# Kernel tuning notes

Measured on AMD Instinct MI355X. Metric: run time of the kernel, lower is better.

Reference implementation:

```python
import jax, jax.numpy as jnp
import numpy as np

N = 50000      # nodes
E = 1600000    # edges
IN = 128       # in_features
OUT = 64       # out_features
H = 2          # heads
ALPHA = 0.2    # LeakyReLU negative slope


def setup_inputs() -> dict:
    key = jax.random.key(0)
    k1, k2, k3, k4 = jax.random.split(key, 4)
    x = jax.random.normal(k1, (N, IN), dtype=jnp.float32)
    edge_index = jax.random.randint(k2, (2, E), 0, N, dtype=jnp.int32)
    # xavier-uniform-ish scaled params
    W = jax.random.normal(k3, (H, IN, OUT), dtype=jnp.float32) / np.float32(np.sqrt(IN))
    a = jax.random.normal(k4, (H, 2 * OUT, 1), dtype=jnp.float32) * np.float32(0.1)
    return {"x": x, "W": W, "a": a, "edge_index": edge_index}


def reference(x, W, a, edge_index):
    src = edge_index[0]
    dst = edge_index[1]
    # per-head linear transform: [N, H, O]
    Wh = jnp.einsum('ni,hio->nho', x, W)
    # split attention vector: a @ [Wh_i || Wh_j] == Wh_i@a_i + Wh_j@a_j
    a_i = a[:, :OUT, 0]   # [H, O]
    a_j = a[:, OUT:, 0]   # [H, O]
    s_i = jnp.einsum('nho,ho->nh', Wh, a_i)   # [N, H]
    s_j = jnp.einsum('nho,ho->nh', Wh, a_j)   # [N, H]
    # per-edge attention logits, LeakyReLU
    e = jax.nn.leaky_relu(s_i[src] + s_j[dst], negative_slope=ALPHA)  # [E, H]
    # faithful to source: GLOBAL softmax over all edges (dim=0) per head
    attn = jax.nn.softmax(e, axis=0)  # [E, H]
    # dropout with rate 0.0 -> identity (eval mode)
    msg = attn[:, :, None] * Wh[dst]  # [E, H, O]
    h = jax.ops.segment_sum(msg, dst, num_segments=N)  # [N, H, O]
    # concat heads along feature dim
    return h.reshape(N, H * OUT)
```

## Files before the change

### kernel.cpp

```cpp
#include <hip/hip_runtime.h>

#define NN 50000
#define EE 1600000
#define INF 128
#define OUTF 64
#define NH 2
#define ALPHA 0.2f

#define NSPREP 391
#define NWPREP 64
#define NBNODE 391

#define HCH 32
#define RNG 8
#define NPR (NN / RNG)
#define EPC (EE / HCH)
#define NI4 (EPC / 4)
#define HWAVES 16
#define WITER ((NI4 + 1023) / 1024)
#define QW 512

typedef __attribute__((ext_vector_type(8))) short s16x8;
typedef __attribute__((ext_vector_type(4))) float f32x4;

__device__ __forceinline__ unsigned short bf16_rne(float f) {
    union { float f; unsigned u; } v; v.f = f;
    unsigned r = v.u + 0x7FFFu + ((v.u >> 16) & 1u);
    return (unsigned short)(r >> 16);
}
__device__ __forceinline__ float bf16_val(unsigned short h) {
    union { unsigned u; float f; } v; v.u = ((unsigned)h) << 16;
    return v.f;
}
__device__ __forceinline__ void split8(const float4 a, const float4 b,
                                       s16x8& hi, s16x8& lo) {
    const float p[8] = {a.x, a.y, a.z, a.w, b.x, b.y, b.z, b.w};
    #pragma unroll
    for (int j = 0; j < 8; ++j) {
        const unsigned short h = bf16_rne(p[j]);
        hi[j] = (short)h;
        lo[j] = (short)bf16_rne(p[j] - bf16_val(h));
    }
}


__global__ __launch_bounds__(256)
void gat_prep(const float* __restrict__ x, const float* __restrict__ Wg,
              const float* __restrict__ av,
              float* __restrict__ si, float* __restrict__ sj,
              unsigned short* __restrict__ Wf, float* __restrict__ Z)
{
    __shared__ float4 u4[128];
    const int tid = threadIdx.x;

    if (blockIdx.x >= NSPREP) {
        const int idx = (blockIdx.x - NSPREP) * 256 + tid;
        if (idx < 2) Z[idx] = 0.0f;
        const int h = idx >> 13;
        const int k = (idx >> 6) & 127;
        const int o = idx & 63;
        const float w = Wg[idx];
        const unsigned short hi = bf16_rne(w);
        const unsigned short lo = bf16_rne(w - bf16_val(hi));
        const int n  = h * 64 + o;
        const int nt = n >> 4;
        const int ks = k >> 5;
        const int kk = k & 31;
        const int ln = (kk >> 3) * 16 + (n & 15);
        const int pos = ((nt * 4 + ks) * 64 + ln) * 8 + (kk & 7);
        Wf[pos] = hi;
        Wf[16384 + pos] = lo;
        return;
    }

    if (tid < 128) {
        const int k = tid;
        float u0 = 0.f, u1 = 0.f, u2 = 0.f, u3 = 0.f;
        #pragma unroll 4
        for (int o = 0; o < 64; o += 4) {
            const float4 w0 = *(const float4*)&Wg[k * 64 + o];
            const float4 w1 = *(const float4*)&Wg[8192 + k * 64 + o];
            const float4 ai0 = *(const float4*)&av[o];
            const float4 aj0 = *(const float4*)&av[64 + o];
            const float4 ai1 = *(const float4*)&av[128 + o];
            const float4 aj1 = *(const float4*)&av[192 + o];
            u0 += w0.x*ai0.x + w0.y*ai0.y + w0.z*ai0.z + w0.w*ai0.w;
            u1 += w0.x*aj0.x + w0.y*aj0.y + w0.z*aj0.z + w0.w*aj0.w;
            u2 += w1.x*ai1.x + w1.y*ai1.y + w1.z*ai1.z + w1.w*ai1.w;
            u3 += w1.x*aj1.x + w1.y*aj1.y + w1.z*aj1.z + w1.w*aj1.w;
        }
        u4[k] = make_float4(u0, u1, u2, u3);
    }
    __syncthreads();

    const int lane = tid & 63;
    const int wv = tid >> 6;
    const int lm = lane & 15;
    const int rsub = lane >> 4;

    #pragma unroll
    for (int p = 0; p < 8; ++p) {
        const int row = blockIdx.x * 128 + p * 16 + wv * 4 + rsub;
        const int rc = row < NN ? row : NN - 1;
        const float4 xa = *(const float4*)(x + (size_t)rc * INF + lm * 8);
        const float4 xb = *(const float4*)(x + (size_t)rc * INF + lm * 8 + 4);
        float s0 = 0.f, s1 = 0.f, s2 = 0.f, s3 = 0.f;
        const float xv[8] = {xa.x, xa.y, xa.z, xa.w, xb.x, xb.y, xb.z, xb.w};
        #pragma unroll
        for (int j = 0; j < 8; ++j) {
            const float4 u = u4[lm * 8 + j];
            s0 = fmaf(xv[j], u.x, s0);
            s1 = fmaf(xv[j], u.y, s1);
            s2 = fmaf(xv[j], u.z, s2);
            s3 = fmaf(xv[j], u.w, s3);
        }
        #pragma unroll
        for (int m = 1; m < 16; m <<= 1) {
            s0 += __shfl_xor(s0, m, 64);
            s1 += __shfl_xor(s1, m, 64);
            s2 += __shfl_xor(s2, m, 64);
            s3 += __shfl_xor(s3, m, 64);
        }
        if (lm == 0 && row < NN) {
            *(float2*)&si[2 * row] = make_float2(s0, s2);
            *(float2*)&sj[2 * row] = make_float2(s1, s3);
        }
    }
}

__global__ __launch_bounds__(1024)
void gat_hist(const int* __restrict__ ei,
              const float* __restrict__ si, const float* __restrict__ sj,
              float* __restrict__ partial, float* __restrict__ Z)
{
    __shared__ float bins[NPR * 2];
    __shared__ unsigned q[HWAVES * QW];
    __shared__ float zr0[HWAVES], zr1[HWAVES];
    const int c = blockIdx.x;
    const int r = blockIdx.y;
    const int nlo = r * NPR;
    const int tid = threadIdx.x;
    const int lane = tid & 63;
    const int wv = tid >> 6;
    const int qbase = wv * QW;

    for (int i = tid; i < NPR; i += 1024)
        ((float2*)bins)[i] = make_float2(0.f, 0.f);
    __syncthreads();

    const int4* src4 = (const int4*)(ei + (size_t)c * EPC);
    const int4* dst4 = (const int4*)(ei + EE + (size_t)c * EPC);

    float z0 = 0.f, z1 = 0.f;
    int qn = 0;

    for (int j = 0; j < WITER; ++j) {
        const int i = j * 1024 + tid;
        int4 d4 = make_int4(-1, -1, -1, -1);
        int4 s4 = make_int4(0, 0, 0, 0);
        if (i < NI4) { d4 = dst4[i]; s4 = src4[i]; }
        const unsigned dd[4] = {(unsigned)d4.x, (unsigned)d4.y,
                                (unsigned)d4.z, (unsigned)d4.w};
        const unsigned ss[4] = {(unsigned)s4.x, (unsigned)s4.y,
                                (unsigned)s4.z, (unsigned)s4.w};

        unsigned rel[4]; bool pass[4];
        #pragma unroll
        for (int k = 0; k < 4; ++k) {
            const unsigned rr = dd[k] / (unsigned)NPR;
            pass[k] = (rr == (unsigned)r);
            rel[k] = dd[k] - rr * (unsigned)NPR;
        }
        unsigned long long m[4];
        #pragma unroll
        for (int k = 0; k < 4; ++k) m[k] = __ballot(pass[k]);

        int cbase = qn;
        #pragma unroll
        for (int k = 0; k < 4; ++k) {
            const unsigned pre = __builtin_amdgcn_mbcnt_hi(
                (unsigned)(m[k] >> 32),
                __builtin_amdgcn_mbcnt_lo((unsigned)(m[k] & 0xffffffffu), 0u));
            if (pass[k])
                q[qbase + cbase + (int)pre] = ss[k] | (rel[k] << 16);
            cbase += __popcll(m[k]);
        }
        qn = cbase;

        if (qn > QW - 256 || j == WITER - 1) {
            for (int t = lane; t < qn; t += 64) {
                const unsigned pk = q[qbase + t];
                const int s = (int)(pk & 0xFFFFu);
                const int rl = (int)(pk >> 16);
                const float2 vi = *(const float2*)&si[2 * s];
                const float2 vj = *(const float2*)&sj[2 * (nlo + rl)];
                float a0 = vi.x + vj.x; a0 = a0 > 0.f ? a0 : ALPHA * a0;
                float a1 = vi.y + vj.y; a1 = a1 > 0.f ? a1 : ALPHA * a1;
                const float w0 = expf(a0);
                const float w1 = expf(a1);
                atomicAdd(&bins[2 * rl], w0);
                atomicAdd(&bins[2 * rl + 1], w1);
                z0 += w0; z1 += w1;
            }
            qn = 0;
        }
    }

    #pragma unroll
    for (int m = 1; m < 64; m <<= 1) {
        z0 += __shfl_xor(z0, m, 64);
        z1 += __shfl_xor(z1, m, 64);
    }
    if (lane == 0) { zr0[wv] = z0; zr1[wv] = z1; }
    __syncthreads();
    if (tid == 0) {
        float t0 = 0.f, t1 = 0.f;
        #pragma unroll
        for (int i = 0; i < HWAVES; ++i) { t0 += zr0[i]; t1 += zr1[i]; }
        atomicAdd(&Z[0], t0);
        atomicAdd(&Z[1], t1);
    }

    float2* P = (float2*)(partial + (size_t)c * 100000 + 2 * nlo);
    for (int i = tid; i < NPR; i += 1024)
        P[i] = ((const float2*)bins)[i];
}

__global__ __launch_bounds__(256)
void gat_node(const float* __restrict__ x, const unsigned short* __restrict__ Wf,
              const float* __restrict__ partial, const float* __restrict__ Z,
              float* __restrict__ out)
{
    __shared__ unsigned short WsL[32768];
    __shared__ float asum[256];
    const int tid = threadIdx.x;
    const int lane = tid & 63;
    const int wv = tid >> 6;
    const int lm = lane & 15;
    const int quad = lane >> 4;

    {
        const float4* gsrc = (const float4*)Wf;
        float4* ldst = (float4*)WsL;
        #pragma unroll
        for (int i = 0; i < 16; ++i)
            ldst[i * 256 + tid] = gsrc[i * 256 + tid];
    }

    {
        const int vbase = blockIdx.x * 256;
        float s = 0.f;
        if (vbase + tid < 2 * NN) {
            #pragma unroll
            for (int cc = 0; cc < HCH; ++cc)
                s += partial[(size_t)cc * 100000 + vbase + tid];
        }
        asum[tid] = s;
    }

    const float rz0 = 1.0f / Z[0];
    const float rz1 = 1.0f / Z[1];

    const int rowA0 = blockIdx.x * 128 + wv * 32 + lm;
    const int rowA1 = rowA0 + 16;
    const int rc0 = rowA0 < NN ? rowA0 : NN - 1;
    const int rc1 = rowA1 < NN ? rowA1 : NN - 1;
    const float* xp0 = x + (size_t)rc0 * INF + quad * 8;
    const float* xp1 = x + (size_t)rc1 * INF + quad * 8;

    f32x4 acc[2][8];
    #pragma unroll
    for (int mi = 0; mi < 2; ++mi)
        #pragma unroll
        for (int nt = 0; nt < 8; ++nt) acc[mi][nt] = (f32x4)0.0f;

    __syncthreads();

    #pragma unroll
    for (int ks = 0; ks < 4; ++ks) {
        s16x8 ah0, al0, ah1, al1;
        {
            const float4 u0 = *(const float4*)(xp0 + ks * 32);
            const float4 v0 = *(const float4*)(xp0 + ks * 32 + 4);
            split8(u0, v0, ah0, al0);
            const float4 u1 = *(const float4*)(xp1 + ks * 32);
            const float4 v1 = *(const float4*)(xp1 + ks * 32 + 4);
            split8(u1, v1, ah1, al1);
        }
        #pragma unroll
        for (int nt = 0; nt < 8; ++nt) {
            const s16x8 bh = *(const s16x8*)&WsL[((nt * 4 + ks) * 64 + lane) * 8];
            const s16x8 bl = *(const s16x8*)&WsL[16384 + ((nt * 4 + ks) * 64 + lane) * 8];
            acc[0][nt] = __builtin_amdgcn_mfma_f32_16x16x32_bf16(ah0, bh, acc[0][nt], 0, 0, 0);
            acc[0][nt] = __builtin_amdgcn_mfma_f32_16x16x32_bf16(ah0, bl, acc[0][nt], 0, 0, 0);
            acc[0][nt] = __builtin_amdgcn_mfma_f32_16x16x32_bf16(al0, bh, acc[0][nt], 0, 0, 0);
            acc[1][nt] = __builtin_amdgcn_mfma_f32_16x16x32_bf16(ah1, bh, acc[1][nt], 0, 0, 0);
            acc[1][nt] = __builtin_amdgcn_mfma_f32_16x16x32_bf16(ah1, bl, acc[1][nt], 0, 0, 0);
            acc[1][nt] = __builtin_amdgcn_mfma_f32_16x16x32_bf16(al1, bh, acc[1][nt], 0, 0, 0);
        }
    }

    #pragma unroll
    for (int mi = 0; mi < 2; ++mi) {
        const int rowoffb = wv * 32 + mi * 16 + quad * 4;
        const int rowb = blockIdx.x * 128 + rowoffb;
        #pragma unroll
        for (int r = 0; r < 4; ++r) {
            const int rr = rowb + r;
            if (rr < NN) {
                const float sc0 = asum[2 * (rowoffb + r)] * rz0;
                const float sc1 = asum[2 * (rowoffb + r) + 1] * rz1;
                float* orow = out + (size_t)rr * (NH * OUTF) + lm;
                #pragma unroll
                for (int nt = 0; nt < 8; ++nt)
                    orow[nt * 16] = acc[mi][nt][r] * (nt < 4 ? sc0 : sc1);
            }
        }
    }
}

extern "C" void kernel_launch(void* const* d_in, const int* in_sizes, int n_in,
                              void* d_out, int out_size, void* d_ws, size_t ws_size,
                              hipStream_t stream)
{
    const float* x = (const float*)d_in[0];
    const float* W = (const float*)d_in[1];
    const float* a = (const float*)d_in[2];
    const int* ei = (const int*)d_in[3];
    float* out = (float*)d_out;
    float* ws = (float*)d_ws;

    float* si = ws;
    float* sj = ws + 100000;
    float* Z = ws + 200000;
    unsigned short* Wf = (unsigned short*)(ws + 200064);
    float* partial = ws + 216448;

    gat_prep<<<dim3(NSPREP + NWPREP), dim3(256), 0, stream>>>(
        x, W, a, si, sj, Wf, Z);

    gat_hist<<<dim3(HCH, RNG), dim3(1024), 0, stream>>>(ei, si, sj, partial, Z);

    gat_node<<<dim3(NBNODE), dim3(256), 0, stream>>>(x, Wf, partial, Z, out);
}
```

Before: 140.9 us.

## Fuse prep, histogram and node kernels into one cooperative kernel with grid syncs

Replaces three separate kernel launches with a single cooperative kernel of 256 blocks of 1024 threads, using grid.sync between the score/weight prep, edge histogram and node GEMM phases. Shared memory is reused across phases through one buffer. This removes the launch gaps and per-kernel ramp-up and tail between stages. In exchange, the prep and node phases now run on only 256 large blocks, which may lower occupancy, and grid-wide barriers add their own cost.

Result: slower. 207.9 us (+47.5%).

```diff
diff --git a/kernel.cpp b/kernel.cpp
--- a/kernel.cpp
+++ b/kernel.cpp
@@ -1,4 +1,5 @@
 #include <hip/hip_runtime.h>
+#include <hip/hip_cooperative_groups.h>
 
 #define NN 50000
 #define EE 1600000
@@ -7,17 +8,16 @@
 #define NH 2
 #define ALPHA 0.2f
 
-#define NSPREP 391
-#define NWPREP 64
-#define NBNODE 391
+#define NBLK 256
+#define NTHR 1024
+#define NWAVE 16
 
 #define HCH 32
 #define RNG 8
 #define NPR (NN / RNG)
 #define EPC (EE / HCH)
 #define NI4 (EPC / 4)
-#define HWAVES 16
-#define WITER ((NI4 + 1023) / 1024)
+#define WITER ((NI4 + NTHR - 1) / NTHR)
 #define QW 512
 
 typedef __attribute__((ext_vector_type(8))) short s16x8;
@@ -44,276 +44,256 @@
 }
 
 
-__global__ __launch_bounds__(256)
-void gat_prep(const float* __restrict__ x, const float* __restrict__ Wg,
-              const float* __restrict__ av,
-              float* __restrict__ si, float* __restrict__ sj,
-              unsigned short* __restrict__ Wf, float* __restrict__ Z)
+__global__ __launch_bounds__(NTHR)
+void gat_fused(const float* __restrict__ x, const float* __restrict__ Wg,
+               const float* __restrict__ av, const int* __restrict__ ei,
+               float* __restrict__ si, float* __restrict__ sj,
+               unsigned short* __restrict__ Wf, float* __restrict__ partial,
+               float* __restrict__ Z, float* __restrict__ out)
 {
-    __shared__ float4 u4[128];
-    const int tid = threadIdx.x;
-
-    if (blockIdx.x >= NSPREP) {
-        const int idx = (blockIdx.x - NSPREP) * 256 + tid;
-        if (idx < 2) Z[idx] = 0.0f;
-        const int h = idx >> 13;
-        const int k = (idx >> 6) & 127;
-        const int o = idx & 63;
-        const float w = Wg[idx];
-        const unsigned short hi = bf16_rne(w);
-        const unsigned short lo = bf16_rne(w - bf16_val(hi));
-        const int n  = h * 64 + o;
-        const int nt = n >> 4;
-        const int ks = k >> 5;
-        const int kk = k & 31;
-        const int ln = (kk >> 3) * 16 + (n & 15);
-        const int pos = ((nt * 4 + ks) * 64 + ln) * 8 + (kk & 7);
-        Wf[pos] = hi;
-        Wf[16384 + pos] = lo;
-        return;
-    }
-
-    if (tid < 128) {
-        const int k = tid;
-        float u0 = 0.f, u1 = 0.f, u2 = 0.f, u3 = 0.f;
-        #pragma unroll 4
-        for (int o = 0; o < 64; o += 4) {
-            const float4 w0 = *(const float4*)&Wg[k * 64 + o];
-            const float4 w1 = *(const float4*)&Wg[8192 + k * 64 + o];
-            const float4 ai0 = *(const float4*)&av[o];
-            const float4 aj0 = *(const float4*)&av[64 + o];
-            const float4 ai1 = *(const float4*)&av[128 + o];
-            const float4 aj1 = *(const float4*)&av[192 + o];
-            u0 += w0.x*ai0.x + w0.y*ai0.y + w0.z*ai0.z + w0.w*ai0.w;
-            u1 += w0.x*aj0.x + w0.y*aj0.y + w0.z*aj0.z + w0.w*aj0.w;
-            u2 += w1.x*ai1.x + w1.y*ai1.y + w1.z*ai1.z + w1.w*ai1.w;
-            u3 += w1.x*aj1.x + w1.y*aj1.y + w1.z*aj1.z + w1.w*aj1.w;
-        }
-        u4[k] = make_float4(u0, u1, u2, u3);
-    }
-    __syncthreads();
-
-    const int lane = tid & 63;
-    const int wv = tid >> 6;
-    const int lm = lane & 15;
-    const int rsub = lane >> 4;
-
-    #pragma unroll
-    for (int p = 0; p < 8; ++p) {
-        const int row = blockIdx.x * 128 + p * 16 + wv * 4 + rsub;
-        const int rc = row < NN ? row : NN - 1;
-        const float4 xa = *(const float4*)(x + (size_t)rc * INF + lm * 8);
-        const float4 xb = *(const float4*)(x + (size_t)rc * INF + lm * 8 + 4);
-        float s0 = 0.f, s1 = 0.f, s2 = 0.f, s3 = 0.f;
-        const float xv[8] = {xa.x, xa.y, xa.z, xa.w, xb.x, xb.y, xb.z, xb.w};
-        #pragma unroll
-        for (int j = 0; j < 8; ++j) {
-            const float4 u = u4[lm * 8 + j];
-            s0 = fmaf(xv[j], u.x, s0);
-            s1 = fmaf(xv[j], u.y, s1);
-            s2 = fmaf(xv[j], u.z, s2);
-            s3 = fmaf(xv[j], u.w, s3);
-        }
-        #pragma unroll
-        for (int m = 1; m < 16; m <<= 1) {
-            s0 += __shfl_xor(s0, m, 64);
-            s1 += __shfl_xor(s1, m, 64);
-            s2 += __shfl_xor(s2, m, 64);
-            s3 += __shfl_xor(s3, m, 64);
-        }
-        if (lm == 0 && row < NN) {
-            *(float2*)&si[2 * row] = make_float2(s0, s2);
-            *(float2*)&sj[2 * row] = make_float2(s1, s3);
-        }
-    }
-}
-
-__global__ __launch_bounds__(1024)
-void gat_hist(const int* __restrict__ ei,
-              const float* __restrict__ si, const float* __restrict__ sj,
-              float* __restrict__ partial, float* __restrict__ Z)
-{
-    __shared__ float bins[NPR * 2];
-    __shared__ unsigned q[HWAVES * QW];
-    __shared__ float zr0[HWAVES], zr1[HWAVES];
-    const int c = blockIdx.x;
-    const int r = blockIdx.y;
-    const int nlo = r * NPR;
+    namespace cg = cooperative_groups;
+    cg::grid_group grid = cg::this_grid();
+
+    __shared__ __align__(16) char smem[83968];
+    __shared__ float zr0[NWAVE], zr1[NWAVE];
+
+    const int bid = blockIdx.x;
     const int tid = threadIdx.x;
     const int lane = tid & 63;
     const int wv = tid >> 6;
-    const int qbase = wv * QW;
-
-    for (int i = tid; i < NPR; i += 1024)
-        ((float2*)bins)[i] = make_float2(0.f, 0.f);
-    __syncthreads();
-
-    const int4* src4 = (const int4*)(ei + (size_t)c * EPC);
-    const int4* dst4 = (const int4*)(ei + EE + (size_t)c * EPC);
-
-    float z0 = 0.f, z1 = 0.f;
-    int qn = 0;
-
-    for (int j = 0; j < WITER; ++j) {
-        const int i = j * 1024 + tid;
-        int4 d4 = make_int4(-1, -1, -1, -1);
-        int4 s4 = make_int4(0, 0, 0, 0);
-        if (i < NI4) { d4 = dst4[i]; s4 = src4[i]; }
-        const unsigned dd[4] = {(unsigned)d4.x, (unsigned)d4.y,
-                                (unsigned)d4.z, (unsigned)d4.w};
-        const unsigned ss[4] = {(unsigned)s4.x, (unsigned)s4.y,
-                                (unsigned)s4.z, (unsigned)s4.w};
-
-        unsigned rel[4]; bool pass[4];
+
+    {
+        float4* u4 = (float4*)smem;
+        if (tid < 128) {
+            const int k = tid;
+            float u0 = 0.f, u1 = 0.f, u2 = 0.f, u3 = 0.f;
+            #pragma unroll 4
+            for (int o = 0; o < 64; o += 4) {
+                const float4 w0 = *(const float4*)&Wg[k * 64 + o];
+                const float4 w1 = *(const float4*)&Wg[8192 + k * 64 + o];
+                const float4 ai0 = *(const float4*)&av[o];
+                const float4 aj0 = *(const float4*)&av[64 + o];
+                const float4 ai1 = *(const float4*)&av[128 + o];
+                const float4 aj1 = *(const float4*)&av[192 + o];
+                u0 += w0.x*ai0.x + w0.y*ai0.y + w0.z*ai0.z + w0.w*ai0.w;
+                u1 += w0.x*aj0.x + w0.y*aj0.y + w0.z*aj0.z + w0.w*aj0.w;
+                u2 += w1.x*ai1.x + w1.y*ai1.y + w1.z*ai1.z + w1.w*ai1.w;
+                u3 += w1.x*aj1.x + w1.y*aj1.y + w1.z*aj1.z + w1.w*aj1.w;
+            }
+            u4[k] = make_float4(u0, u1, u2, u3);
+        }
+        __syncthreads();
+
+        if (bid * 256 < NN) {
+            const int lm = lane & 15;
+            const int rsub = lane >> 4;
+            #pragma unroll
+            for (int p = 0; p < 4; ++p) {
+                const int row = bid * 256 + wv * 16 + p * 4 + rsub;
+                const int rc = row < NN ? row : NN - 1;
+                const float4 xa = *(const float4*)(x + (size_t)rc * INF + lm * 8);
+                const float4 xb = *(const float4*)(x + (size_t)rc * INF + lm * 8 + 4);
+                float s0 = 0.f, s1 = 0.f, s2 = 0.f, s3 = 0.f;
+                const float xv[8] = {xa.x, xa.y, xa.z, xa.w, xb.x, xb.y, xb.z, xb.w};
+                #pragma unroll
+                for (int j = 0; j < 8; ++j) {
+                    const float4 u = u4[lm * 8 + j];
+                    s0 = fmaf(xv[j], u.x, s0);
+                    s1 = fmaf(xv[j], u.y, s1);
+                    s2 = fmaf(xv[j], u.z, s2);
+                    s3 = fmaf(xv[j], u.w, s3);
+                }
+                #pragma unroll
+                for (int m = 1; m < 16; m <<= 1) {
+                    s0 += __shfl_xor(s0, m, 64);
+                    s1 += __shfl_xor(s1, m, 64);
+                    s2 += __shfl_xor(s2, m, 64);
+                    s3 += __shfl_xor(s3, m, 64);
+                }
+                if (lm == 0 && row < NN) {
+                    *(float2*)&si[2 * row] = make_float2(s0, s2);
+                    *(float2*)&sj[2 * row] = make_float2(s1, s3);
+                }
+            }
+        }
+
+        if (bid < 16) {
+            const int idx = bid * 1024 + tid;
+            const int h = idx >> 13;
+            const int k = (idx >> 6) & 127;
+            const int o = idx & 63;
+            const float w = Wg[idx];
+            const unsigned short hi = bf16_rne(w);
+            const unsigned short lo = bf16_rne(w - bf16_val(hi));
+            const int n  = h * 64 + o;
+            const int nt = n >> 4;
+            const int ks = k >> 5;
+            const int kk = k & 31;
+            const int ln = (kk >> 3) * 16 + (n & 15);
+            const int pos = ((nt * 4 + ks) * 64 + ln) * 8 + (kk & 7);
+            Wf[pos] = hi;
+            Wf[16384 + pos] = lo;
+        }
+        if (bid == 0 && tid < 2) Z[tid] = 0.0f;
+    }
+
+    grid.sync();
+
+    {
+        float* bins = (float*)smem;
+        unsigned* q = (unsigned*)(smem + 50000);
+        const int c = bid & 31;
+        const int r = bid >> 5;
+        const int nlo = r * NPR;
+        const int qbase = wv * QW;
+
+        for (int i = tid; i < NPR; i += NTHR)
+            ((float2*)bins)[i] = make_float2(0.f, 0.f);
+        __syncthreads();
+
+        const int4* src4 = (const int4*)(ei + (size_t)c * EPC);
+        const int4* dst4 = (const int4*)(ei + EE + (size_t)c * EPC);
+
+        float z0 = 0.f, z1 = 0.f;
+        int qn = 0;
+
+        for (int j = 0; j < WITER; ++j) {
+            const int i = j * NTHR + tid;
+            int4 d4 = make_int4(-1, -1, -1, -1);
+            int4 s4 = make_int4(0, 0, 0, 0);
+            if (i < NI4) { d4 = dst4[i]; s4 = src4[i]; }
+            const unsigned dd[4] = {(unsigned)d4.x, (unsigned)d4.y,
+                                    (unsigned)d4.z, (unsigned)d4.w};
+            const unsigned ss[4] = {(unsigned)s4.x, (unsigned)s4.y,
+                                    (unsigned)s4.z, (unsigned)s4.w};
+
+            unsigned rel[4]; bool pass[4];
+            #pragma unroll
+            for (int k = 0; k < 4; ++k) {
+                const unsigned rr = dd[k] / (unsigned)NPR;
+                pass[k] = (rr == (unsigned)r);
+                rel[k] = dd[k] - rr * (unsigned)NPR;
+            }
+            unsigned long long m[4];
+            #pragma unroll
+            for (int k = 0; k < 4; ++k) m[k] = __ballot(pass[k]);
+
+            int cbase = qn;
+            #pragma unroll
+            for (int k = 0; k < 4; ++k) {
+                const unsigned pre = __builtin_amdgcn_mbcnt_hi(
+                    (unsigned)(m[k] >> 32),
+                    __builtin_amdgcn_mbcnt_lo((unsigned)(m[k] & 0xffffffffu), 0u));
+                if (pass[k])
+                    q[qbase + cbase + (int)pre] = ss[k] | (rel[k] << 16);
+                cbase += __popcll(m[k]);
+            }
+            qn = cbase;
+
+            if (qn > QW - 256 || j == WITER - 1) {
+                for (int t = lane; t < qn; t += 64) {
+                    const unsigned pk = q[qbase + t];
+                    const int s = (int)(pk & 0xFFFFu);
+                    const int rl = (int)(pk >> 16);
+                    const float2 vi = *(const float2*)&si[2 * s];
+                    const float2 vj = *(const float2*)&sj[2 * (nlo + rl)];
+                    float a0 = vi.x + vj.x; a0 = a0 > 0.f ? a0 : ALPHA * a0;
+                    float a1 = vi.y + vj.y; a1 = a1 > 0.f ? a1 : ALPHA * a1;
+                    const float w0 = expf(a0);
+                    const float w1 = expf(a1);
+                    atomicAdd(&bins[2 * rl], w0);
+                    atomicAdd(&bins[2 * rl + 1], w1);
+                    z0 += w0; z1 += w1;
+                }
+                qn = 0;
+            }
+        }
+
         #pragma unroll
-        for (int k = 0; k < 4; ++k) {
-            const unsigned rr = dd[k] / (unsigned)NPR;
-            pass[k] = (rr == (unsigned)r);
-            rel[k] = dd[k] - rr * (unsigned)NPR;
-        }
-        unsigned long long m[4];
-        #pragma unroll
-        for (int k = 0; k < 4; ++k) m[k] = __ballot(pass[k]);
-
-        int cbase = qn;
-        #pragma unroll
-        for (int k = 0; k < 4; ++k) {
-            const unsigned pre = __builtin_amdgcn_mbcnt_hi(
-                (unsigned)(m[k] >> 32),
-                __builtin_amdgcn_mbcnt_lo((unsigned)(m[k] & 0xffffffffu), 0u));
-            if (pass[k])
-                q[qbase + cbase + (int)pre] = ss[k] | (rel[k] << 16);
-            cbase += __popcll(m[k]);
-        }
-        qn = cbase;
-
-        if (qn > QW - 256 || j == WITER - 1) {
-            for (int t = lane; t < qn; t += 64) {
-                const unsigned pk = q[qbase + t];
-                const int s = (int)(pk & 0xFFFFu);
-                const int rl = (int)(pk >> 16);
-                const float2 vi = *(const float2*)&si[2 * s];
-                const float2 vj = *(const float2*)&sj[2 * (nlo + rl)];
-                float a0 = vi.x + vj.x; a0 = a0 > 0.f ? a0 : ALPHA * a0;
-                float a1 = vi.y + vj.y; a1 = a1 > 0.f ? a1 : ALPHA * a1;
-                const float w0 = expf(a0);
-                const float w1 = expf(a1);
-                atomicAdd(&bins[2 * rl], w0);
-                atomicAdd(&bins[2 * rl + 1], w1);
-                z0 += w0; z1 += w1;
-            }
-            qn = 0;
-        }
+        for (int m = 1; m < 64; m <<= 1) {
+            z0 += __shfl_xor(z0, m, 64);
+            z1 += __shfl_xor(z1, m, 64);
+        }
+        if (lane == 0) { zr0[wv] = z0; zr1[wv] = z1; }
+        __syncthreads();
+        if (tid == 0) {
+            float t0 = 0.f, t1 = 0.f;
+            #pragma unroll
+            for (int i = 0; i < NWAVE; ++i) { t0 += zr0[i]; t1 += zr1[i]; }
+            atomicAdd(&Z[0], t0);
+            atomicAdd(&Z[1], t1);
+        }
+
+        float2* P = (float2*)(partial + (size_t)c * 100000 + 2 * nlo);
+        for (int i = tid; i < NPR; i += NTHR)
+            P[i] = ((const float2*)bins)[i];
     }
 
-    #pragma unroll
-    for (int m = 1; m < 64; m <<= 1) {
-        z0 += __shfl_xor(z0, m, 64);
-        z1 += __shfl_xor(z1, m, 64);
-    }
-    if (lane == 0) { zr0[wv] = z0; zr1[wv] = z1; }
-    __syncthreads();
-    if (tid == 0) {
-        float t0 = 0.f, t1 = 0.f;
-        #pragma unroll
-        for (int i = 0; i < HWAVES; ++i) { t0 += zr0[i]; t1 += zr1[i]; }
-        atomicAdd(&Z[0], t0);
-        atomicAdd(&Z[1], t1);
-    }
-
-    float2* P = (float2*)(partial + (size_t)c * 100000 + 2 * nlo);
-    for (int i = tid; i < NPR; i += 1024)
-        P[i] = ((const float2*)bins)[i];
-}
-
-__global__ __launch_bounds__(256)
-void gat_node(const float* __restrict__ x, const unsigned short* __restrict__ Wf,
-              const float* __restrict__ partial, const float* __restrict__ Z,
-              float* __restrict__ out)
-{
-    __shared__ unsigned short WsL[32768];
-    __shared__ float asum[256];
-    const int tid = threadIdx.x;
-    const int lane = tid & 63;
-    const int wv = tid >> 6;
-    const int lm = lane & 15;
-    const int quad = lane >> 4;
+    grid.sync();
 
     {
-        const float4* gsrc = (const float4*)Wf;
-        float4* ldst = (float4*)WsL;
-        #pragma unroll
-        for (int i = 0; i < 16; ++i)
-            ldst[i * 256 + tid] = gsrc[i * 256 + tid];
-    }
-
-    {
-        const int vbase = blockIdx.x * 256;
-        float s = 0.f;
-        if (vbase + tid < 2 * NN) {
-            #pragma unroll
-            for (int cc = 0; cc < HCH; ++cc)
-                s += partial[(size_t)cc * 100000 + vbase + tid];
-        }
-        asum[tid] = s;
-    }
-
-    const float rz0 = 1.0f / Z[0];
-    const float rz1 = 1.0f / Z[1];
-
-    const int rowA0 = blockIdx.x * 128 + wv * 32 + lm;
-    const int rowA1 = rowA0 + 16;
-    const int rc0 = rowA0 < NN ? rowA0 : NN - 1;
-    const int rc1 = rowA1 < NN ? rowA1 : NN - 1;
-    const float* xp0 = x + (size_t)rc0 * INF + quad * 8;
-    const float* xp1 = x + (size_t)rc1 * INF + quad * 8;
-
-    f32x4 acc[2][8];
-    #pragma unroll
-    for (int mi = 0; mi < 2; ++mi)
-        #pragma unroll
-        for (int nt = 0; nt < 8; ++nt) acc[mi][nt] = (f32x4)0.0f;
-
-    __syncthreads();
-
-    #pragma unroll
-    for (int ks = 0; ks < 4; ++ks) {
-        s16x8 ah0, al0, ah1, al1;
+        unsigned short* Ws = (unsigned short*)smem;
+        float* asum = (float*)(smem + 65536);
+
         {
-            const float4 u0 = *(const float4*)(xp0 + ks * 32);
-            const float4 v0 = *(const float4*)(xp0 + ks * 32 + 4);
-            split8(u0, v0, ah0, al0);
-            const float4 u1 = *(const float4*)(xp1 + ks * 32);
-            const float4 v1 = *(const float4*)(xp1 + ks * 32 + 4);
-            split8(u1, v1, ah1, al1);
-        }
-        #pragma unroll
-        for (int nt = 0; nt < 8; ++nt) {
-            const s16x8 bh = *(const s16x8*)&WsL[((nt * 4 + ks) * 64 + lane) * 8];
-            const s16x8 bl = *(const s16x8*)&WsL[16384 + ((nt * 4 + ks) * 64 + lane) * 8];
-            acc[0][nt] = __builtin_amdgcn_mfma_f32_16x16x32_bf16(ah0, bh, acc[0][nt], 0, 0, 0);
-            acc[0][nt] = __builtin_amdgcn_mfma_f32_16x16x32_bf16(ah0, bl, acc[0][nt], 0, 0, 0);
-            acc[0][nt] = __builtin_amdgcn_mfma_f32_16x16x32_bf16(al0, bh, acc[0][nt], 0, 0, 0);
-            acc[1][nt] = __builtin_amdgcn_mfma_f32_16x16x32_bf16(ah1, bh, acc[1][nt], 0, 0, 0);
-            acc[1][nt] = __builtin_amdgcn_mfma_f32_16x16x32_bf16(ah1, bl, acc[1][nt], 0, 0, 0);
-            acc[1][nt] = __builtin_amdgcn_mfma_f32_16x16x32_bf16(al1, bh, acc[1][nt], 0, 0, 0);
-        }
-    }
-
-    #pragma unroll
-    for (int mi = 0; mi < 2; ++mi) {
-        const int rowoffb = wv * 32 + mi * 16 + quad * 4;
-        const int rowb = blockIdx.x * 128 + rowoffb;
-        #pragma unroll
-        for (int r = 0; r < 4; ++r) {
-            const int rr = rowb + r;
-            if (rr < NN) {
-                const float sc0 = asum[2 * (rowoffb + r)] * rz0;
-                const float sc1 = asum[2 * (rowoffb + r) + 1] * rz1;
+            const float4* gsrc = (const float4*)Wf;
+            float4* ldst = (float4*)Ws;
+            #pragma unroll
+            for (int i = 0; i < 4; ++i)
+                ldst[i * 1024 + tid] = gsrc[i * 1024 + tid];
+        }
+
+        if (tid < 512) {
+            const int vb = bid * 512 + tid;
+            float s = 0.f;
+            if (vb < 2 * NN) {
+                #pragma unroll
+                for (int cc = 0; cc < HCH; ++cc)
+                    s += partial[(size_t)cc * 100000 + vb];
+            }
+            asum[tid] = s;
+        }
+        __syncthreads();
+
+        const float rz0 = 1.0f / Z[0];
+        const float rz1 = 1.0f / Z[1];
+
+        const int w0 = bid * 256 + wv * 16;
+        if (w0 < NN) {
+            const int lm = lane & 15;
+            const int quad = lane >> 4;
+            const float* xp = x + (size_t)(w0 + lm) * INF + quad * 8;
+
+            f32x4 acc[8];
+            #pragma unroll
+            for (int nt = 0; nt < 8; ++nt) acc[nt] = (f32x4)0.0f;
+
+            #pragma unroll
+            for (int ks = 0; ks < 4; ++ks) {
+                s16x8 ah, al;
+                const float4 u = *(const float4*)(xp + ks * 32);
+                const float4 v = *(const float4*)(xp + ks * 32 + 4);
+                split8(u, v, ah, al);
+                #pragma unroll
+                for (int nt = 0; nt < 8; ++nt) {
+                    const s16x8 bh = *(const s16x8*)&Ws[((nt * 4 + ks) * 64 + lane) * 8];
+                    const s16x8 bl = *(const s16x8*)&Ws[16384 + ((nt * 4 + ks) * 64 + lane) * 8];
+                    acc[nt] = __builtin_amdgcn_mfma_f32_16x16x32_bf16(ah, bh, acc[nt], 0, 0, 0);
+                    acc[nt] = __builtin_amdgcn_mfma_f32_16x16x32_bf16(ah, bl, acc[nt], 0, 0, 0);
+                    acc[nt] = __builtin_amdgcn_mfma_f32_16x16x32_bf16(al, bh, acc[nt], 0, 0, 0);
+                }
+            }
+
+            const int lrow0 = wv * 16 + quad * 4;
+            #pragma unroll
+            for (int r = 0; r < 4; ++r) {
+                const int rr = bid * 256 + lrow0 + r;
+                const float sc0 = asum[2 * (lrow0 + r)] * rz0;
+                const float sc1 = asum[2 * (lrow0 + r) + 1] * rz1;
                 float* orow = out + (size_t)rr * (NH * OUTF) + lm;
                 #pragma unroll
                 for (int nt = 0; nt < 8; ++nt)
-                    orow[nt * 16] = acc[mi][nt][r] * (nt < 4 ? sc0 : sc1);
+                    orow[nt * 16] = acc[nt][r] * (nt < 4 ? sc0 : sc1);
             }
         }
     }
@@ -336,10 +316,9 @@
     unsigned short* Wf = (unsigned short*)(ws + 200064);
     float* partial = ws + 216448;
 
-    gat_prep<<<dim3(NSPREP + NWPREP), dim3(256), 0, stream>>>(
-        x, W, a, si, sj, Wf, Z);
-
-    gat_hist<<<dim3(HCH, RNG), dim3(1024), 0, stream>>>(ei, si, sj, partial, Z);
-
-    gat_node<<<dim3(NBNODE), dim3(256), 0, stream>>>(x, Wf, partial, Z, out);
-}
+    void* args[] = { (void*)&x, (void*)&W, (void*)&a, (void*)&ei,
+                     (void*)&si, (void*)&sj, (void*)&Wf, (void*)&partial,
+                     (void*)&Z, (void*)&out };
+    hipLaunchCooperativeKernel((const void*)gat_fused, dim3(NBLK), dim3(NTHR),
+                               args, 0, stream);
+}
```

## Prefetch next edge indices, replace division with range check, double hist chunks

Applied to the files above, without the earlier changes.

The histogram kernel now issues the global loads for the next iteration's edge indices before processing the current batch. This hides load latency behind the ballot, compaction and drain work. The per-edge integer division that found the destination range is replaced by a single unsigned subtract-and-compare against this block's node range. The edge dimension is split into twice as many chunks, each handled by 512-thread blocks, to give more blocks and better latency tolerance. In exchange, the partial-sum buffer doubles, so the node kernel reads and reduces twice as many partials per node.

After: 147.1 us. +4.4%, slower.

```diff
diff --git a/kernel.cpp b/kernel.cpp
--- a/kernel.cpp
+++ b/kernel.cpp
@@ -11,13 +11,13 @@
 #define NWPREP 64
 #define NBNODE 391
 
-#define HCH 32
+#define HCH 64
 #define RNG 8
 #define NPR (NN / RNG)
 #define EPC (EE / HCH)
 #define NI4 (EPC / 4)
-#define HWAVES 16
-#define WITER ((NI4 + 1023) / 1024)
+#define HWAVES 8
+#define WITER ((NI4 + 511) / 512)
 #define QW 512
 
 typedef __attribute__((ext_vector_type(8))) short s16x8;
@@ -128,7 +128,23 @@
     }
 }
 
-__global__ __launch_bounds__(1024)
+#define DRAIN_Q                                                         \
+    for (int t = lane; t < qn; t += 64) {                               \
+        const unsigned pk = q[qbase + t];                               \
+        const int s = (int)(pk & 0xFFFFu);                              \
+        const int rl = (int)(pk >> 16);                                 \
+        const float2 vi = *(const float2*)&si[2 * s];                   \
+        const float2 vj = *(const float2*)&sj[2 * (nlo + rl)];          \
+        float a0 = vi.x + vj.x; a0 = a0 > 0.f ? a0 : ALPHA * a0;        \
+        float a1 = vi.y + vj.y; a1 = a1 > 0.f ? a1 : ALPHA * a1;        \
+        const float w0 = expf(a0);                                      \
+        const float w1 = expf(a1);                                      \
+        atomicAdd(&bins[2 * rl], w0);                                   \
+        atomicAdd(&bins[2 * rl + 1], w1);                               \
+        z0 += w0; z1 += w1;                                             \
+    }
+
+__global__ __launch_bounds__(512)
 void gat_hist(const int* __restrict__ ei,
               const float* __restrict__ si, const float* __restrict__ sj,
               float* __restrict__ partial, float* __restrict__ Z)
@@ -139,12 +155,13 @@
     const int c = blockIdx.x;
     const int r = blockIdx.y;
     const int nlo = r * NPR;
+    const unsigned nlo_u = (unsigned)nlo;
     const int tid = threadIdx.x;
     const int lane = tid & 63;
     const int wv = tid >> 6;
     const int qbase = wv * QW;
 
-    for (int i = tid; i < NPR; i += 1024)
+    for (int i = tid; i < NPR; i += 512)
         ((float2*)bins)[i] = make_float2(0.f, 0.f);
     __syncthreads();
 
@@ -154,57 +171,45 @@
     float z0 = 0.f, z1 = 0.f;
     int qn = 0;
 
+    int4 d4 = make_int4(-1, -1, -1, -1);
+    int4 s4 = make_int4(0, 0, 0, 0);
+    if (tid < NI4) { d4 = dst4[tid]; s4 = src4[tid]; }
+
     for (int j = 0; j < WITER; ++j) {
-        const int i = j * 1024 + tid;
-        int4 d4 = make_int4(-1, -1, -1, -1);
-        int4 s4 = make_int4(0, 0, 0, 0);
-        if (i < NI4) { d4 = dst4[i]; s4 = src4[i]; }
+        int4 d4n = make_int4(-1, -1, -1, -1);
+        int4 s4n = make_int4(0, 0, 0, 0);
+        const int inx = (j + 1) * 512 + tid;
+        if (j + 1 < WITER && inx < NI4) { d4n = dst4[inx]; s4n = src4[inx]; }
+
+        if (qn >= QW - 256) {
+            DRAIN_Q;
+            qn = 0;
+        }
+
         const unsigned dd[4] = {(unsigned)d4.x, (unsigned)d4.y,
                                 (unsigned)d4.z, (unsigned)d4.w};
         const unsigned ss[4] = {(unsigned)s4.x, (unsigned)s4.y,
                                 (unsigned)s4.z, (unsigned)s4.w};
 
-        unsigned rel[4]; bool pass[4];
+        int cbase = qn;
         #pragma unroll
         for (int k = 0; k < 4; ++k) {
-            const unsigned rr = dd[k] / (unsigned)NPR;
-            pass[k] = (rr == (unsigned)r);
-            rel[k] = dd[k] - rr * (unsigned)NPR;
-        }
-        unsigned long long m[4];
-        #pragma unroll
-        for (int k = 0; k < 4; ++k) m[k] = __ballot(pass[k]);
-
-        int cbase = qn;
-        #pragma unroll
-        for (int k = 0; k < 4; ++k) {
+            const unsigned rel = dd[k] - nlo_u;
+            const bool pass = rel < (unsigned)NPR;
+            const unsigned long long m = __ballot(pass);
             const unsigned pre = __builtin_amdgcn_mbcnt_hi(
-                (unsigned)(m[k] >> 32),
-                __builtin_amdgcn_mbcnt_lo((unsigned)(m[k] & 0xffffffffu), 0u));
-            if (pass[k])
-                q[qbase + cbase + (int)pre] = ss[k] | (rel[k] << 16);
-            cbase += __popcll(m[k]);
+                (unsigned)(m >> 32),
+                __builtin_amdgcn_mbcnt_lo((unsigned)(m & 0xffffffffu), 0u));
+            if (pass)
+                q[qbase + cbase + (int)pre] = ss[k] | (rel << 16);
+            cbase += __popcll(m);
         }
         qn = cbase;
 
-        if (qn > QW - 256 || j == WITER - 1) {
-            for (int t = lane; t < qn; t += 64) {
-                const unsigned pk = q[qbase + t];
-                const int s = (int)(pk & 0xFFFFu);
-                const int rl = (int)(pk >> 16);
-                const float2 vi = *(const float2*)&si[2 * s];
-                const float2 vj = *(const float2*)&sj[2 * (nlo + rl)];
-                float a0 = vi.x + vj.x; a0 = a0 > 0.f ? a0 : ALPHA * a0;
-                float a1 = vi.y + vj.y; a1 = a1 > 0.f ? a1 : ALPHA * a1;
-                const float w0 = expf(a0);
-                const float w1 = expf(a1);
-                atomicAdd(&bins[2 * rl], w0);
-                atomicAdd(&bins[2 * rl + 1], w1);
-                z0 += w0; z1 += w1;
-            }
-            qn = 0;
-        }
-    }
+        d4 = d4n; s4 = s4n;
+    }
+
+    DRAIN_Q;
 
     #pragma unroll
     for (int m = 1; m < 64; m <<= 1) {
@@ -222,7 +227,7 @@
     }
 
     float2* P = (float2*)(partial + (size_t)c * 100000 + 2 * nlo);
-    for (int i = tid; i < NPR; i += 1024)
+    for (int i = tid; i < NPR; i += 512)
         P[i] = ((const float2*)bins)[i];
 }
 
@@ -251,7 +256,6 @@
         const int vbase = blockIdx.x * 256;
         float s = 0.f;
         if (vbase + tid < 2 * NN) {
-            #pragma unroll
             for (int cc = 0; cc < HCH; ++cc)
                 s += partial[(size_t)cc * 100000 + vbase + tid];
         }
@@ -339,7 +343,7 @@
     gat_prep<<<dim3(NSPREP + NWPREP), dim3(256), 0, stream>>>(
         x, W, a, si, sj, Wf, Z);
 
-    gat_hist<<<dim3(HCH, RNG), dim3(1024), 0, stream>>>(ei, si, sj, partial, Z);
+    gat_hist<<<dim3(HCH, RNG), dim3(512), 0, stream>>>(ei, si, sj, partial, Z);
 
     gat_node<<<dim3(NBNODE), dim3(256), 0, stream>>>(x, Wf, partial, Z, out);
 }
```
